# Optimization experiments

Measured on AMD Instinct MI355X. Metric: run time of the kernel, lower is better.

The kernel has to match this reference:

```python
import jax, jax.numpy as jnp
import numpy as np
from jax.ops import segment_sum

NUM_EMBEDDINGS = 512
EMBEDDING_DIM = 64
COMMITMENT_COST = 0.25
DECAY = 0.99
EPSILON = 1e-05


def setup_inputs() -> dict:
    key = jax.random.key(0)
    k1, k2, k3 = jax.random.split(key, 3)
    B, C, T = 32, EMBEDDING_DIM, 4096
    z = jax.random.normal(k1, (B, C, T), dtype=jnp.float32)
    embedding = jax.random.normal(k2, (NUM_EMBEDDINGS, EMBEDDING_DIM), dtype=jnp.float32)
    cluster_size = jnp.zeros((NUM_EMBEDDINGS,), dtype=jnp.float32)
    embed_avg = jax.random.normal(k3, (NUM_EMBEDDINGS, EMBEDDING_DIM), dtype=jnp.float32)
    return {"z": z, "embedding": embedding, "cluster_size": cluster_size, "embed_avg": embed_avg}


def reference(z, embedding, cluster_size, embed_avg):
    B, C, T = z.shape
    K = embedding.shape[0]
    # flatten: (B, C, T) -> (B*T, C), matching reshape(B,C,-1).permute(0,2,1).reshape(-1,C)
    z_flat = jnp.transpose(z, (0, 2, 1)).reshape(-1, C)  # [N, C]
    N = z_flat.shape[0]

    # squared-euclidean nearest-code search (argmin of cdist == argmin of sq dist)
    d2 = (jnp.sum(z_flat * z_flat, axis=1, keepdims=True)
          - 2.0 * (z_flat @ embedding.T)
          + jnp.sum(embedding * embedding, axis=1)[None, :])  # [N, K]
    indices = jnp.argmin(d2, axis=1)  # [N] int

    # quantize: gather instead of one-hot matmul (same math)
    quantized_flat = embedding[indices]  # [N, C]
    quantized = jnp.transpose(quantized_flat.reshape(B, T, C), (0, 2, 1))  # [B, C, T]

    # EMA codebook update (training branch)
    n = segment_sum(jnp.ones((N,), dtype=z.dtype), indices, num_segments=K)  # [K]
    new_cluster_size = cluster_size * DECAY + (1.0 - DECAY) * n
    embed_sum = segment_sum(z_flat, indices, num_segments=K)  # [K, C]
    new_embed_avg = embed_avg * DECAY + (1.0 - DECAY) * embed_sum
    n_tot = jnp.sum(new_cluster_size)
    cs_smoothed = (new_cluster_size + EPSILON) / (n_tot + K * EPSILON) * n_tot
    new_embedding = new_embed_avg / cs_smoothed[:, None]

    # commitment loss against detached quantized
    commitment_loss = jnp.mean((z - jax.lax.stop_gradient(quantized)) ** 2)
    vq_loss = COMMITMENT_COST * commitment_loss

    # straight-through estimator
    quantized_st = z + jax.lax.stop_gradient(quantized - z)

    # perplexity over code usage (zero-count codes contribute ~0, as in torch unique version)
    probs = n / N
    perplexity = jnp.exp(-jnp.sum(probs * jnp.log(probs + 1e-10)))

    return (quantized_st, indices, vq_loss, perplexity,
            new_embedding, new_cluster_size, new_embed_avg)
```

## Files before the change

kernel.cpp:

```cpp
#include <hip/hip_runtime.h>
#include <math.h>

#define KB_NUM 512
#define DIMC 64
#define BSZ 32
#define TLEN 4096
#define NTOK (BSZ * TLEN)
#define DECAY_F 0.99f
#define EPS_F 1e-5f

#define Q_OFF    ((size_t)0)
#define IDX_OFF  ((size_t)BSZ * DIMC * TLEN)
#define LOSS_OFF (IDX_OFF + (size_t)NTOK)
#define PLEX_OFF (LOSS_OFF + 1)
#define NEMB_OFF (PLEX_OFF + 1)
#define NCS_OFF  (NEMB_OFF + (size_t)KB_NUM * DIMC)
#define NEA_OFF  (NCS_OFF + (size_t)KB_NUM)

typedef _Float16 f16x8 __attribute__((ext_vector_type(8)));
typedef float    f32x4 __attribute__((ext_vector_type(4)));

__global__ __launch_bounds__(64) void vq_prep_e(
    const float* __restrict__ emb,
    _Float16* __restrict__ efrag,
    float* __restrict__ enorm)
{
    const int k = blockIdx.x;
    const int c = threadIdx.x;
    float v = emb[(size_t)k * DIMC + c];
    _Float16 h = (_Float16)v;
    _Float16 l = (_Float16)(v - (float)h);

    const int kgrp = k >> 4, row = k & 15;
    const int ks = c >> 5, seg = (c & 31) >> 3, j = c & 7;
    const int lane = seg * 16 + row;
    const size_t base = ((size_t)(kgrp * 2 + ks) * 2) * 512;
    efrag[base + (size_t)lane * 8 + j]       = h;
    efrag[base + 512 + (size_t)lane * 8 + j] = l;

    float s = v * v;
    #pragma unroll
    for (int off = 32; off > 0; off >>= 1)
        s += __shfl_down(s, off, 64);
    if (c == 0) enorm[k] = 0.5f * s;
}

#define LOADA(P, kg) do {                                                     \
    const _Float16* fb_ = efrag + ((size_t)((kg) & 31) * 4) * 512             \
                                + (size_t)ln * 8;                             \
    P##h0 = *(const f16x8*)(fb_);                                             \
    P##l0 = *(const f16x8*)(fb_ + 512);                                       \
    P##h1 = *(const f16x8*)(fb_ + 1024);                                      \
    P##l1 = *(const f16x8*)(fb_ + 1536);                                      \
} while (0)

#define CONSUME(P, ct) do {                                                   \
    _Pragma("unroll")                                                         \
    for (int tt = 0; tt < 4; ++tt)                                            \
        acc[ct][tt] = __builtin_amdgcn_mfma_f32_16x16x32_f16(                 \
            P##h0, zhf[tt][0], acc[ct][tt], 0, 0, 0);                         \
    _Pragma("unroll")                                                         \
    for (int tt = 0; tt < 4; ++tt)                                            \
        acc[ct][tt] = __builtin_amdgcn_mfma_f32_16x16x32_f16(                 \
            P##h0, zlf[tt][0], acc[ct][tt], 0, 0, 0);                         \
    _Pragma("unroll")                                                         \
    for (int tt = 0; tt < 4; ++tt)                                            \
        acc[ct][tt] = __builtin_amdgcn_mfma_f32_16x16x32_f16(                 \
            P##l0, zhf[tt][0], acc[ct][tt], 0, 0, 0);                         \
    _Pragma("unroll")                                                         \
    for (int tt = 0; tt < 4; ++tt)                                            \
        acc[ct][tt] = __builtin_amdgcn_mfma_f32_16x16x32_f16(                 \
            P##l0, zlf[tt][0], acc[ct][tt], 0, 0, 0);                         \
    _Pragma("unroll")                                                         \
    for (int tt = 0; tt < 4; ++tt)                                            \
        acc[ct][tt] = __builtin_amdgcn_mfma_f32_16x16x32_f16(                 \
            P##h1, zhf[tt][1], acc[ct][tt], 0, 0, 0);                         \
    _Pragma("unroll")                                                         \
    for (int tt = 0; tt < 4; ++tt)                                            \
        acc[ct][tt] = __builtin_amdgcn_mfma_f32_16x16x32_f16(                 \
            P##h1, zlf[tt][1], acc[ct][tt], 0, 0, 0);                         \
    _Pragma("unroll")                                                         \
    for (int tt = 0; tt < 4; ++tt)                                            \
        acc[ct][tt] = __builtin_amdgcn_mfma_f32_16x16x32_f16(                 \
            P##l1, zhf[tt][1], acc[ct][tt], 0, 0, 0);                         \
    _Pragma("unroll")                                                         \
    for (int tt = 0; tt < 4; ++tt)                                            \
        acc[ct][tt] = __builtin_amdgcn_mfma_f32_16x16x32_f16(                 \
            P##l1, zlf[tt][1], acc[ct][tt], 0, 0, 0);                         \
} while (0)

__global__ __launch_bounds__(256, 2) void vq_main_kernel(
    const float* __restrict__ z,
    const float* __restrict__ emb,
    const _Float16* __restrict__ efrag,
    const float* __restrict__ enorm,
    float* __restrict__ out,
    float* __restrict__ lossAcc)
{
    __shared__ float zs[256 * 65];

    const int tid = threadIdx.x;
    const int w   = tid >> 6;
    const int ln  = tid & 63;
    const int bk  = blockIdx.x;
    const int b   = bk >> 4;
    const int t0  = (bk & 15) << 8;

    const float* zg = z + (size_t)b * (DIMC * TLEN) + t0;

    #pragma unroll 8
    for (int c = 0; c < DIMC; ++c)
        zs[tid * 65 + c] = zg[(size_t)c * TLEN + tid];
    __syncthreads();

    f16x8 zhf[4][2], zlf[4][2];
    #pragma unroll
    for (int tt = 0; tt < 4; ++tt) {
        #pragma unroll
        for (int ks = 0; ks < 2; ++ks) {
            const float* zrow = &zs[(w * 64 + tt * 16 + (ln & 15)) * 65
                                    + ks * 32 + ((ln >> 4) << 3)];
            #pragma unroll
            for (int j = 0; j < 8; ++j) {
                float v = zrow[j];
                _Float16 h = (_Float16)v;
                zhf[tt][ks][j] = h;
                zlf[tt][ks][j] = (_Float16)(v - (float)h);
            }
        }
    }

    float bv[4] = {3.4e38f, 3.4e38f, 3.4e38f, 3.4e38f};
    int   bi[4] = {0, 0, 0, 0};

    f16x8 A0h0, A0l0, A0h1, A0l1;
    f16x8 A1h0, A1l0, A1h1, A1l1;
    LOADA(A0, 0);
    LOADA(A1, 1);

    #pragma unroll 1
    for (int chunk = 0; chunk < 8; ++chunk) {
        const int kb = chunk * 4;
        f32x4 acc[4][4];
        #pragma unroll
        for (int ct = 0; ct < 4; ++ct)
            #pragma unroll
            for (int tt = 0; tt < 4; ++tt)
                acc[ct][tt] = (f32x4){0.f, 0.f, 0.f, 0.f};

        CONSUME(A0, 0); LOADA(A0, kb + 2);
        CONSUME(A1, 1); LOADA(A1, kb + 3);
        CONSUME(A0, 2); LOADA(A0, kb + 4);
        CONSUME(A1, 3); LOADA(A1, kb + 5);

        #pragma unroll
        for (int ct = 0; ct < 4; ++ct) {
            const int cb = chunk * 64 + ct * 16 + ((ln >> 4) << 2);
            float4 en = *(const float4*)(enorm + cb);
            const float e0 = en.x, e1 = en.y, e2 = en.z, e3 = en.w;
            #pragma unroll
            for (int tt = 0; tt < 4; ++tt) {
                float s0 = e0 - acc[ct][tt][0];
                float s1 = e1 - acc[ct][tt][1];
                float s2 = e2 - acc[ct][tt][2];
                float s3 = e3 - acc[ct][tt][3];
                if (s0 < bv[tt]) { bv[tt] = s0; bi[tt] = cb; }
                if (s1 < bv[tt]) { bv[tt] = s1; bi[tt] = cb + 1; }
                if (s2 < bv[tt]) { bv[tt] = s2; bi[tt] = cb + 2; }
                if (s3 < bv[tt]) { bv[tt] = s3; bi[tt] = cb + 3; }
            }
        }
    }

    #pragma unroll
    for (int mask = 16; mask <= 32; mask <<= 1) {
        #pragma unroll
        for (int tt = 0; tt < 4; ++tt) {
            float ov = __shfl_xor(bv[tt], mask, 64);
            int   oi = __shfl_xor(bi[tt], mask, 64);
            if (ov < bv[tt] || (ov == bv[tt] && oi < bi[tt])) {
                bv[tt] = ov; bi[tt] = oi;
            }
        }
    }

    const int g = ln >> 4;
    const int idxv = (g == 0) ? bi[0] : (g == 1) ? bi[1] : (g == 2) ? bi[2] : bi[3];
    const int tok = w * 64 + ln;

    out[IDX_OFF + (size_t)b * TLEN + t0 + tok] = (float)idxv;

    const float* er   = emb + (size_t)idxv * DIMC;
    const float* zrow = &zs[tok * 65];
    float* qo = out + (size_t)b * (DIMC * TLEN) + t0 + tok;

    float lsum = 0.f;
    #pragma unroll
    for (int c4 = 0; c4 < DIMC / 4; ++c4) {
        float4 ev = *(const float4*)(er + c4 * 4);
        float z0 = zrow[c4 * 4 + 0], z1 = zrow[c4 * 4 + 1];
        float z2 = zrow[c4 * 4 + 2], z3 = zrow[c4 * 4 + 3];
        float d0 = ev.x - z0, d1 = ev.y - z1, d2 = ev.z - z2, d3 = ev.w - z3;
        qo[(size_t)(c4 * 4 + 0) * TLEN] = z0 + d0;
        qo[(size_t)(c4 * 4 + 1) * TLEN] = z1 + d1;
        qo[(size_t)(c4 * 4 + 2) * TLEN] = z2 + d2;
        qo[(size_t)(c4 * 4 + 3) * TLEN] = z3 + d3;
        lsum = fmaf(d0, d0, lsum); lsum = fmaf(d1, d1, lsum);
        lsum = fmaf(d2, d2, lsum); lsum = fmaf(d3, d3, lsum);
    }

    #pragma unroll
    for (int off = 32; off > 0; off >>= 1)
        lsum += __shfl_down(lsum, off, 64);
    if (ln == 0) atomicAdd(lossAcc, lsum);
}

__global__ __launch_bounds__(512, 1) void vq_bin_kernel(
    const float* __restrict__ z,
    const float* __restrict__ out,
    float* __restrict__ cnt,
    float* __restrict__ esum,
    int R)
{
    __shared__ float acc[KB_NUM][DIMC + 1];
    __shared__ float scnt[KB_NUM];

    const int tid = threadIdx.x;
    for (int j = tid; j < KB_NUM * (DIMC + 1); j += 512) ((float*)acc)[j] = 0.f;
    scnt[tid] = 0.f;
    __syncthreads();

    const int gt = blockIdx.x * 512 + tid;
    const int b  = gt >> 12;
    const int t  = gt & (TLEN - 1);
    const int idx = (int)out[IDX_OFF + gt];
    atomicAdd(&scnt[idx], 1.0f);

    const float* zp = z + (size_t)b * (DIMC * TLEN) + t;
    #pragma unroll 16
    for (int c = 0; c < DIMC; ++c) {
        float zv = zp[(size_t)c * TLEN];
        atomicAdd(&acc[idx][c], zv);
    }
    __syncthreads();

    const int r = (int)((unsigned)blockIdx.x % (unsigned)R);
    for (int j = tid; j < KB_NUM * DIMC; j += 512) {
        const int k = j >> 6, c = j & 63;
        float v = acc[k][c];
        if (v != 0.f) atomicAdd(esum + (size_t)r * (KB_NUM * DIMC) + j, v);
    }
    {
        float v = scnt[tid];
        if (v != 0.f) atomicAdd(cnt + (size_t)r * KB_NUM + tid, v);
    }
}

__global__ __launch_bounds__(512) void vq_stats_kernel(
    const float* __restrict__ cluster_size,
    const float* __restrict__ cnt,
    const float* __restrict__ lossAcc,
    float* __restrict__ out,
    float* __restrict__ ntotp,
    int R)
{
    const int k = threadIdx.x;

    float n = 0.f;
    #pragma unroll 4
    for (int r = 0; r < R; ++r) n += cnt[(size_t)r * KB_NUM + k];

    float ncs = cluster_size[k] * DECAY_F + (1.0f - DECAY_F) * n;
    out[NCS_OFF + k] = ncs;

    __shared__ float red[KB_NUM];

    red[k] = ncs;
    __syncthreads();
    for (int s = KB_NUM / 2; s > 0; s >>= 1) {
        if (k < s) red[k] += red[k + s];
        __syncthreads();
    }
    if (k == 0) ntotp[0] = red[0];
    __syncthreads();

    float p = n * (1.0f / (float)NTOK);
    red[k] = p * logf(p + 1e-10f);
    __syncthreads();
    for (int s = KB_NUM / 2; s > 0; s >>= 1) {
        if (k < s) red[k] += red[k + s];
        __syncthreads();
    }
    if (k == 0) {
        out[PLEX_OFF] = expf(-red[0]);
        out[LOSS_OFF] = 0.25f * lossAcc[0] * (1.0f / (float)(BSZ * DIMC * TLEN));
    }
}

__global__ __launch_bounds__(64) void vq_embed_kernel(
    const float* __restrict__ embed_avg,
    const float* __restrict__ esum,
    const float* __restrict__ ntotp,
    float* __restrict__ out,
    int R)
{
    const int k = blockIdx.x;
    const int c = threadIdx.x;

    float es = 0.f;
    #pragma unroll 4
    for (int r = 0; r < R; ++r)
        es += esum[((size_t)r * KB_NUM + k) * DIMC + c];

    float nea = embed_avg[(size_t)k * DIMC + c] * DECAY_F + (1.0f - DECAY_F) * es;
    out[NEA_OFF + (size_t)k * DIMC + c] = nea;

    float ncs  = out[NCS_OFF + k];
    float ntot = ntotp[0];
    float denom = (ncs + EPS_F) / (ntot + (float)KB_NUM * EPS_F) * ntot;
    out[NEMB_OFF + (size_t)k * DIMC + c] = nea / denom;
}

extern "C" void kernel_launch(void* const* d_in, const int* in_sizes, int n_in,
                              void* d_out, int out_size, void* d_ws, size_t ws_size,
                              hipStream_t stream)
{
    const float* z            = (const float*)d_in[0];
    const float* emb          = (const float*)d_in[1];
    const float* cluster_size = (const float*)d_in[2];
    const float* embed_avg    = (const float*)d_in[3];
    float* out = (float*)d_out;

    char* ws = (char*)d_ws;
    float*     lossAcc = (float*)ws;
    float*     ntotp   = (float*)(ws + 64);
    float*     enorm   = (float*)(ws + 256);
    _Float16*  efrag   = (_Float16*)(ws + 4096);
    const size_t CNT_OFF = 4096 + 131072;
    const size_t perR = (size_t)(KB_NUM + KB_NUM * DIMC) * sizeof(float);

    int R = 1;
    if (ws_size > CNT_OFF + perR)
        R = (int)((ws_size - CNT_OFF) / perR);
    if (R < 1) R = 1;
    if (R > 16) R = 16;

    float* cnt  = (float*)(ws + CNT_OFF);
    float* esum = cnt + (size_t)R * KB_NUM;

    hipMemsetAsync(ws, 0, CNT_OFF + (size_t)R * perR, stream);

    vq_prep_e<<<dim3(KB_NUM), dim3(DIMC), 0, stream>>>(emb, efrag, enorm);

    vq_main_kernel<<<dim3(NTOK / 256), dim3(256), 0, stream>>>(
        z, emb, efrag, enorm, out, lossAcc);

    vq_bin_kernel<<<dim3(NTOK / 512), dim3(512), 0, stream>>>(z, out, cnt, esum, R);

    vq_stats_kernel<<<dim3(1), dim3(512), 0, stream>>>(
        cluster_size, cnt, lossAcc, out, ntotp, R);

    vq_embed_kernel<<<dim3(KB_NUM), dim3(DIMC), 0, stream>>>(
        embed_avg, esum, ntotp, out, R);
}
```

Baseline: 134.9 us.

## Halve tokens per block in VQ main kernel to raise occupancy

Each block now handles 128 tokens instead of 256, with each wave covering 32 tokens, so the grid doubles and per-thread accumulator and fragment registers halve. Launch bounds move to 4 blocks per SM and shared memory per block halves. The epilogue is split so two lanes share one token, each handling half the channels. The cost is that every codebook fragment load now feeds half as many MFMAs, so global/L2 traffic for the codebook doubles relative to compute.

```diff
diff --git a/kernel.cpp b/kernel.cpp
--- a/kernel.cpp
+++ b/kernel.cpp
@@ -8,6 +8,7 @@
 #define NTOK (BSZ * TLEN)
 #define DECAY_F 0.99f
 #define EPS_F 1e-5f
+#define MTOK 128
 
 #define Q_OFF    ((size_t)0)
 #define IDX_OFF  ((size_t)BSZ * DIMC * TLEN)
@@ -56,40 +57,40 @@
 
 #define CONSUME(P, ct) do {                                                   \
     _Pragma("unroll")                                                         \
-    for (int tt = 0; tt < 4; ++tt)                                            \
+    for (int tt = 0; tt < 2; ++tt)                                            \
         acc[ct][tt] = __builtin_amdgcn_mfma_f32_16x16x32_f16(                 \
             P##h0, zhf[tt][0], acc[ct][tt], 0, 0, 0);                         \
     _Pragma("unroll")                                                         \
-    for (int tt = 0; tt < 4; ++tt)                                            \
+    for (int tt = 0; tt < 2; ++tt)                                            \
         acc[ct][tt] = __builtin_amdgcn_mfma_f32_16x16x32_f16(                 \
             P##h0, zlf[tt][0], acc[ct][tt], 0, 0, 0);                         \
     _Pragma("unroll")                                                         \
-    for (int tt = 0; tt < 4; ++tt)                                            \
+    for (int tt = 0; tt < 2; ++tt)                                            \
         acc[ct][tt] = __builtin_amdgcn_mfma_f32_16x16x32_f16(                 \
             P##l0, zhf[tt][0], acc[ct][tt], 0, 0, 0);                         \
     _Pragma("unroll")                                                         \
-    for (int tt = 0; tt < 4; ++tt)                                            \
+    for (int tt = 0; tt < 2; ++tt)                                            \
         acc[ct][tt] = __builtin_amdgcn_mfma_f32_16x16x32_f16(                 \
             P##l0, zlf[tt][0], acc[ct][tt], 0, 0, 0);                         \
     _Pragma("unroll")                                                         \
-    for (int tt = 0; tt < 4; ++tt)                                            \
+    for (int tt = 0; tt < 2; ++tt)                                            \
         acc[ct][tt] = __builtin_amdgcn_mfma_f32_16x16x32_f16(                 \
             P##h1, zhf[tt][1], acc[ct][tt], 0, 0, 0);                         \
     _Pragma("unroll")                                                         \
-    for (int tt = 0; tt < 4; ++tt)                                            \
+    for (int tt = 0; tt < 2; ++tt)                                            \
         acc[ct][tt] = __builtin_amdgcn_mfma_f32_16x16x32_f16(                 \
             P##h1, zlf[tt][1], acc[ct][tt], 0, 0, 0);                         \
     _Pragma("unroll")                                                         \
-    for (int tt = 0; tt < 4; ++tt)                                            \
+    for (int tt = 0; tt < 2; ++tt)                                            \
         acc[ct][tt] = __builtin_amdgcn_mfma_f32_16x16x32_f16(                 \
             P##l1, zhf[tt][1], acc[ct][tt], 0, 0, 0);                         \
     _Pragma("unroll")                                                         \
-    for (int tt = 0; tt < 4; ++tt)                                            \
+    for (int tt = 0; tt < 2; ++tt)                                            \
         acc[ct][tt] = __builtin_amdgcn_mfma_f32_16x16x32_f16(                 \
             P##l1, zlf[tt][1], acc[ct][tt], 0, 0, 0);                         \
 } while (0)
 
-__global__ __launch_bounds__(256, 2) void vq_main_kernel(
+__global__ __launch_bounds__(256, 4) void vq_main_kernel(
     const float* __restrict__ z,
     const float* __restrict__ emb,
     const _Float16* __restrict__ efrag,
@@ -97,28 +98,32 @@
     float* __restrict__ out,
     float* __restrict__ lossAcc)
 {
-    __shared__ float zs[256 * 65];
+    __shared__ float zs[MTOK * 65];
 
     const int tid = threadIdx.x;
     const int w   = tid >> 6;
     const int ln  = tid & 63;
     const int bk  = blockIdx.x;
-    const int b   = bk >> 4;
-    const int t0  = (bk & 15) << 8;
+    const int b   = bk >> 5;
+    const int t0  = (bk & 31) << 7;
 
     const float* zg = z + (size_t)b * (DIMC * TLEN) + t0;
 
-    #pragma unroll 8
-    for (int c = 0; c < DIMC; ++c)
-        zs[tid * 65 + c] = zg[(size_t)c * TLEN + tid];
-    __syncthreads();
-
-    f16x8 zhf[4][2], zlf[4][2];
-    #pragma unroll
-    for (int tt = 0; tt < 4; ++tt) {
+    {
+        const int tok   = tid & (MTOK - 1);
+        const int chalf = (tid >> 7) * 32;
+        #pragma unroll 8
+        for (int j = 0; j < 32; ++j)
+            zs[tok * 65 + chalf + j] = zg[(size_t)(chalf + j) * TLEN + tok];
+    }
+    __syncthreads();
+
+    f16x8 zhf[2][2], zlf[2][2];
+    #pragma unroll
+    for (int tt = 0; tt < 2; ++tt) {
         #pragma unroll
         for (int ks = 0; ks < 2; ++ks) {
-            const float* zrow = &zs[(w * 64 + tt * 16 + (ln & 15)) * 65
+            const float* zrow = &zs[(w * 32 + tt * 16 + (ln & 15)) * 65
                                     + ks * 32 + ((ln >> 4) << 3)];
             #pragma unroll
             for (int j = 0; j < 8; ++j) {
@@ -130,8 +135,8 @@
         }
     }
 
-    float bv[4] = {3.4e38f, 3.4e38f, 3.4e38f, 3.4e38f};
-    int   bi[4] = {0, 0, 0, 0};
+    float bv[2] = {3.4e38f, 3.4e38f};
+    int   bi[2] = {0, 0};
 
     f16x8 A0h0, A0l0, A0h1, A0l1;
     f16x8 A1h0, A1l0, A1h1, A1l1;
@@ -141,11 +146,11 @@
     #pragma unroll 1
     for (int chunk = 0; chunk < 8; ++chunk) {
         const int kb = chunk * 4;
-        f32x4 acc[4][4];
+        f32x4 acc[4][2];
         #pragma unroll
         for (int ct = 0; ct < 4; ++ct)
             #pragma unroll
-            for (int tt = 0; tt < 4; ++tt)
+            for (int tt = 0; tt < 2; ++tt)
                 acc[ct][tt] = (f32x4){0.f, 0.f, 0.f, 0.f};
 
         CONSUME(A0, 0); LOADA(A0, kb + 2);
@@ -159,7 +164,7 @@
             float4 en = *(const float4*)(enorm + cb);
             const float e0 = en.x, e1 = en.y, e2 = en.z, e3 = en.w;
             #pragma unroll
-            for (int tt = 0; tt < 4; ++tt) {
+            for (int tt = 0; tt < 2; ++tt) {
                 float s0 = e0 - acc[ct][tt][0];
                 float s1 = e1 - acc[ct][tt][1];
                 float s2 = e2 - acc[ct][tt][2];
@@ -175,7 +180,7 @@
     #pragma unroll
     for (int mask = 16; mask <= 32; mask <<= 1) {
         #pragma unroll
-        for (int tt = 0; tt < 4; ++tt) {
+        for (int tt = 0; tt < 2; ++tt) {
             float ov = __shfl_xor(bv[tt], mask, 64);
             int   oi = __shfl_xor(bi[tt], mask, 64);
             if (ov < bv[tt] || (ov == bv[tt] && oi < bi[tt])) {
@@ -184,19 +189,21 @@
         }
     }
 
-    const int g = ln >> 4;
-    const int idxv = (g == 0) ? bi[0] : (g == 1) ? bi[1] : (g == 2) ? bi[2] : bi[3];
-    const int tok = w * 64 + ln;
-
-    out[IDX_OFF + (size_t)b * TLEN + t0 + tok] = (float)idxv;
-
-    const float* er   = emb + (size_t)idxv * DIMC;
-    const float* zrow = &zs[tok * 65];
-    float* qo = out + (size_t)b * (DIMC * TLEN) + t0 + tok;
+    const int tte   = ln >> 5;
+    const int idxv  = tte ? bi[1] : bi[0];
+    const int tok   = w * 32 + tte * 16 + (ln & 15);
+    const int chalf = ((ln >> 4) & 1) * 32;
+
+    if (((ln >> 4) & 1) == 0)
+        out[IDX_OFF + (size_t)b * TLEN + t0 + tok] = (float)idxv;
+
+    const float* er   = emb + (size_t)idxv * DIMC + chalf;
+    const float* zrow = &zs[tok * 65 + chalf];
+    float* qo = out + (size_t)b * (DIMC * TLEN) + t0 + tok + (size_t)chalf * TLEN;
 
     float lsum = 0.f;
     #pragma unroll
-    for (int c4 = 0; c4 < DIMC / 4; ++c4) {
+    for (int c4 = 0; c4 < 8; ++c4) {
         float4 ev = *(const float4*)(er + c4 * 4);
         float z0 = zrow[c4 * 4 + 0], z1 = zrow[c4 * 4 + 1];
         float z2 = zrow[c4 * 4 + 2], z3 = zrow[c4 * 4 + 3];
@@ -352,7 +359,7 @@
 
     vq_prep_e<<<dim3(KB_NUM), dim3(DIMC), 0, stream>>>(emb, efrag, enorm);
 
-    vq_main_kernel<<<dim3(NTOK / 256), dim3(256), 0, stream>>>(
+    vq_main_kernel<<<dim3(NTOK / MTOK), dim3(256), 0, stream>>>(
         z, emb, efrag, enorm, out, lossAcc);
 
     vq_bin_kernel<<<dim3(NTOK / 512), dim3(512), 0, stream>>>(z, out, cnt, esum, R);
```

Result: slower. 157.4 us (+16.7%).

## Stage z tiles in LDS for binning and cache code norms in shared memory

Applied to the files above, without the earlier changes.

The binning kernel now loads 64-token tiles of z into LDS and then walks them token by token. Each wavefront's 64 lanes do atomic adds across the 64 channels of a single code row, instead of each thread scattering atomics to random code rows. This removes bank conflicts and same-address contention in the LDS atomics, at the cost of extra barriers and staging per chunk. Separately, the main kernel copies the 512 code norms into shared memory once per block and reads them from there instead of from global memory inside the argmin loop.

```diff
diff --git a/kernel.cpp b/kernel.cpp
--- a/kernel.cpp
+++ b/kernel.cpp
@@ -98,6 +98,7 @@
     float* __restrict__ lossAcc)
 {
     __shared__ float zs[256 * 65];
+    __shared__ float sen[KB_NUM];
 
     const int tid = threadIdx.x;
     const int w   = tid >> 6;
@@ -105,6 +106,9 @@
     const int bk  = blockIdx.x;
     const int b   = bk >> 4;
     const int t0  = (bk & 15) << 8;
+
+    sen[tid]       = enorm[tid];
+    sen[tid + 256] = enorm[tid + 256];
 
     const float* zg = z + (size_t)b * (DIMC * TLEN) + t0;
 
@@ -156,7 +160,7 @@
         #pragma unroll
         for (int ct = 0; ct < 4; ++ct) {
             const int cb = chunk * 64 + ct * 16 + ((ln >> 4) << 2);
-            float4 en = *(const float4*)(enorm + cb);
+            float4 en = *(const float4*)&sen[cb];
             const float e0 = en.x, e1 = en.y, e2 = en.z, e3 = en.w;
             #pragma unroll
             for (int tt = 0; tt < 4; ++tt) {
@@ -223,26 +227,48 @@
     int R)
 {
     __shared__ float acc[KB_NUM][DIMC + 1];
+    __shared__ float zs[64][DIMC + 1];
     __shared__ float scnt[KB_NUM];
+    __shared__ int   idxbuf[64];
 
     const int tid = threadIdx.x;
+    const int w   = tid >> 6;
+    const int ln  = tid & 63;
+
     for (int j = tid; j < KB_NUM * (DIMC + 1); j += 512) ((float*)acc)[j] = 0.f;
-    scnt[tid] = 0.f;
-    __syncthreads();
-
-    const int gt = blockIdx.x * 512 + tid;
-    const int b  = gt >> 12;
-    const int t  = gt & (TLEN - 1);
-    const int idx = (int)out[IDX_OFF + gt];
-    atomicAdd(&scnt[idx], 1.0f);
-
-    const float* zp = z + (size_t)b * (DIMC * TLEN) + t;
-    #pragma unroll 16
-    for (int c = 0; c < DIMC; ++c) {
-        float zv = zp[(size_t)c * TLEN];
-        atomicAdd(&acc[idx][c], zv);
-    }
-    __syncthreads();
+    if (tid < KB_NUM) scnt[tid] = 0.f;
+    __syncthreads();
+
+    const int b   = blockIdx.x >> 3;
+    const int tb  = (blockIdx.x & 7) * 512;
+    const float* zp = z + (size_t)b * (DIMC * TLEN) + tb;
+    const size_t gib = IDX_OFF + (size_t)b * TLEN + tb;
+
+    #pragma unroll 1
+    for (int ch = 0; ch < 8; ++ch) {
+        const int t0 = ch * 64;
+        {
+            const int cb = w * 8;
+            #pragma unroll
+            for (int j = 0; j < 8; ++j) {
+                const int c = cb + j;
+                zs[ln][c] = zp[(size_t)c * TLEN + t0 + ln];
+            }
+            if (tid < 64)
+                idxbuf[tid] = (int)out[gib + t0 + tid];
+        }
+        __syncthreads();
+
+        #pragma unroll
+        for (int i = 0; i < 8; ++i) {
+            const int tok = w * 8 + i;
+            const int idx = idxbuf[tok];
+            float v = zs[tok][ln];
+            atomicAdd(&acc[idx][ln], v);
+            if (ln == 0) atomicAdd(&scnt[idx], 1.0f);
+        }
+        __syncthreads();
+    }
 
     const int r = (int)((unsigned)blockIdx.x % (unsigned)R);
     for (int j = tid; j < KB_NUM * DIMC; j += 512) {
@@ -250,7 +276,7 @@
         float v = acc[k][c];
         if (v != 0.f) atomicAdd(esum + (size_t)r * (KB_NUM * DIMC) + j, v);
     }
-    {
+    if (tid < KB_NUM) {
         float v = scnt[tid];
         if (v != 0.f) atomicAdd(cnt + (size_t)r * KB_NUM + tid, v);
     }
```

New measurement: 141.3 us. +4.8%, slower.

## Write per-block partial codebook sums instead of global atomics; cache norms in LDS

Applied to the files above, without the earlier changes.

The binning kernel now writes each block's per-code sums and counts to its own partial buffer (256 partitions) with plain stores instead of global float atomics. The stats and embed kernels then reduce across all partitions. The shared accumulator is transposed to [C][K+1], and the main kernel stages the codebook norms in shared memory. This removes global atomic contention and the large memset, at the cost of writing and reading about 32 MB of partials plus a long serial reduction loop in the embed kernel.

```diff
diff --git a/kernel.cpp b/kernel.cpp
--- a/kernel.cpp
+++ b/kernel.cpp
@@ -8,6 +8,7 @@
 #define NTOK (BSZ * TLEN)
 #define DECAY_F 0.99f
 #define EPS_F 1e-5f
+#define NPART 256
 
 #define Q_OFF    ((size_t)0)
 #define IDX_OFF  ((size_t)BSZ * DIMC * TLEN)
@@ -98,6 +99,7 @@
     float* __restrict__ lossAcc)
 {
     __shared__ float zs[256 * 65];
+    __shared__ float sen[KB_NUM];
 
     const int tid = threadIdx.x;
     const int w   = tid >> 6;
@@ -105,6 +107,9 @@
     const int bk  = blockIdx.x;
     const int b   = bk >> 4;
     const int t0  = (bk & 15) << 8;
+
+    sen[tid]       = enorm[tid];
+    sen[tid + 256] = enorm[tid + 256];
 
     const float* zg = z + (size_t)b * (DIMC * TLEN) + t0;
 
@@ -156,7 +161,7 @@
         #pragma unroll
         for (int ct = 0; ct < 4; ++ct) {
             const int cb = chunk * 64 + ct * 16 + ((ln >> 4) << 2);
-            float4 en = *(const float4*)(enorm + cb);
+            float4 en = *(const float4*)&sen[cb];
             const float e0 = en.x, e1 = en.y, e2 = en.z, e3 = en.w;
             #pragma unroll
             for (int tt = 0; tt < 4; ++tt) {
@@ -215,60 +220,62 @@
     if (ln == 0) atomicAdd(lossAcc, lsum);
 }
 
+template <bool ATOMICFLUSH>
 __global__ __launch_bounds__(512, 1) void vq_bin_kernel(
     const float* __restrict__ z,
     const float* __restrict__ out,
-    float* __restrict__ cnt,
-    float* __restrict__ esum,
-    int R)
-{
-    __shared__ float acc[KB_NUM][DIMC + 1];
+    float* __restrict__ pcnt,
+    float* __restrict__ pesum)
+{
+    __shared__ float accT[DIMC][KB_NUM + 1];
     __shared__ float scnt[KB_NUM];
 
     const int tid = threadIdx.x;
-    for (int j = tid; j < KB_NUM * (DIMC + 1); j += 512) ((float*)acc)[j] = 0.f;
+    for (int j = tid; j < DIMC * (KB_NUM + 1); j += 512) ((float*)accT)[j] = 0.f;
     scnt[tid] = 0.f;
     __syncthreads();
 
-    const int gt = blockIdx.x * 512 + tid;
-    const int b  = gt >> 12;
-    const int t  = gt & (TLEN - 1);
-    const int idx = (int)out[IDX_OFF + gt];
-    atomicAdd(&scnt[idx], 1.0f);
-
-    const float* zp = z + (size_t)b * (DIMC * TLEN) + t;
-    #pragma unroll 16
+    const int b  = blockIdx.x >> 3;
+    const int tb = (blockIdx.x & 7) * 512;
+    const int myidx = (int)out[IDX_OFF + (size_t)b * TLEN + tb + tid];
+    atomicAdd(&scnt[myidx], 1.0f);
+
+    const float* zp = z + (size_t)b * (DIMC * TLEN) + tb;
+    #pragma unroll 8
     for (int c = 0; c < DIMC; ++c) {
-        float zv = zp[(size_t)c * TLEN];
-        atomicAdd(&acc[idx][c], zv);
-    }
-    __syncthreads();
-
-    const int r = (int)((unsigned)blockIdx.x % (unsigned)R);
+        float v = zp[(size_t)c * TLEN + tid];
+        atomicAdd(&accT[c][myidx], v);
+    }
+    __syncthreads();
+
+    float* pe = pesum + (size_t)blockIdx.x * (KB_NUM * DIMC);
     for (int j = tid; j < KB_NUM * DIMC; j += 512) {
         const int k = j >> 6, c = j & 63;
-        float v = acc[k][c];
-        if (v != 0.f) atomicAdd(esum + (size_t)r * (KB_NUM * DIMC) + j, v);
-    }
-    {
+        float v = accT[c][k];
+        if (ATOMICFLUSH) { if (v != 0.f) atomicAdd(pe + j, v); }
+        else             pe[j] = v;
+    }
+    if (ATOMICFLUSH) {
         float v = scnt[tid];
-        if (v != 0.f) atomicAdd(cnt + (size_t)r * KB_NUM + tid, v);
+        if (v != 0.f) atomicAdd(pcnt + tid, v);
+    } else {
+        pcnt[(size_t)blockIdx.x * KB_NUM + tid] = scnt[tid];
     }
 }
 
 __global__ __launch_bounds__(512) void vq_stats_kernel(
     const float* __restrict__ cluster_size,
-    const float* __restrict__ cnt,
+    const float* __restrict__ pcnt,
     const float* __restrict__ lossAcc,
     float* __restrict__ out,
     float* __restrict__ ntotp,
-    int R)
+    int P)
 {
     const int k = threadIdx.x;
 
     float n = 0.f;
-    #pragma unroll 4
-    for (int r = 0; r < R; ++r) n += cnt[(size_t)r * KB_NUM + k];
+    #pragma unroll 8
+    for (int p = 0; p < P; ++p) n += pcnt[(size_t)p * KB_NUM + k];
 
     float ncs = cluster_size[k] * DECAY_F + (1.0f - DECAY_F) * n;
     out[NCS_OFF + k] = ncs;
@@ -299,18 +306,18 @@
 
 __global__ __launch_bounds__(64) void vq_embed_kernel(
     const float* __restrict__ embed_avg,
-    const float* __restrict__ esum,
+    const float* __restrict__ pesum,
     const float* __restrict__ ntotp,
     float* __restrict__ out,
-    int R)
+    int P)
 {
     const int k = blockIdx.x;
     const int c = threadIdx.x;
 
     float es = 0.f;
-    #pragma unroll 4
-    for (int r = 0; r < R; ++r)
-        es += esum[((size_t)r * KB_NUM + k) * DIMC + c];
+    #pragma unroll 16
+    for (int p = 0; p < P; ++p)
+        es += pesum[(size_t)p * (KB_NUM * DIMC) + (size_t)k * DIMC + c];
 
     float nea = embed_avg[(size_t)k * DIMC + c] * DECAY_F + (1.0f - DECAY_F) * es;
     out[NEA_OFF + (size_t)k * DIMC + c] = nea;
@@ -336,30 +343,41 @@
     float*     ntotp   = (float*)(ws + 64);
     float*     enorm   = (float*)(ws + 256);
     _Float16*  efrag   = (_Float16*)(ws + 4096);
-    const size_t CNT_OFF = 4096 + 131072;
-    const size_t perR = (size_t)(KB_NUM + KB_NUM * DIMC) * sizeof(float);
-
-    int R = 1;
-    if (ws_size > CNT_OFF + perR)
-        R = (int)((ws_size - CNT_OFF) / perR);
-    if (R < 1) R = 1;
-    if (R > 16) R = 16;
-
-    float* cnt  = (float*)(ws + CNT_OFF);
-    float* esum = cnt + (size_t)R * KB_NUM;
-
-    hipMemsetAsync(ws, 0, CNT_OFF + (size_t)R * perR, stream);
+    const size_t PART_OFF   = 4096 + 131072;
+    const size_t pcnt_bytes  = (size_t)NPART * KB_NUM * sizeof(float);
+    const size_t pesum_bytes = (size_t)NPART * KB_NUM * DIMC * sizeof(float);
+    const size_t need = PART_OFF + pcnt_bytes + pesum_bytes;
+
+    int P;
+    float *pcnt, *pesum;
+    if (ws_size >= need) {
+        P = NPART;
+        pcnt  = (float*)(ws + PART_OFF);
+        pesum = (float*)(ws + PART_OFF + pcnt_bytes);
+        hipMemsetAsync(ws, 0, 4096, stream);
+    } else {
+        P = 1;
+        pcnt  = (float*)(ws + PART_OFF);
+        pesum = (float*)(ws + PART_OFF + KB_NUM * sizeof(float));
+        hipMemsetAsync(ws, 0, PART_OFF + (KB_NUM + KB_NUM * DIMC) * sizeof(float),
+                       stream);
+    }
 
     vq_prep_e<<<dim3(KB_NUM), dim3(DIMC), 0, stream>>>(emb, efrag, enorm);
 
     vq_main_kernel<<<dim3(NTOK / 256), dim3(256), 0, stream>>>(
         z, emb, efrag, enorm, out, lossAcc);
 
-    vq_bin_kernel<<<dim3(NTOK / 512), dim3(512), 0, stream>>>(z, out, cnt, esum, R);
+    if (P == NPART)
+        vq_bin_kernel<false><<<dim3(NTOK / 512), dim3(512), 0, stream>>>(
+            z, out, pcnt, pesum);
+    else
+        vq_bin_kernel<true><<<dim3(NTOK / 512), dim3(512), 0, stream>>>(
+            z, out, pcnt, pesum);
 
     vq_stats_kernel<<<dim3(1), dim3(512), 0, stream>>>(
-        cluster_size, cnt, lossAcc, out, ntotp, R);
+        cluster_size, pcnt, lossAcc, out, ntotp, P);
 
     vq_embed_kernel<<<dim3(KB_NUM), dim3(DIMC), 0, stream>>>(
-        embed_avg, esum, ntotp, out, R);
-}
+        embed_avg, pesum, ntotp, out, P);
+}
```

Result: slower. 157.7 us (+16.9%).
